# Kernel tuning notes

Hardware: AMD Instinct MI355X
Metric: run time of the kernel (lower is better)

## Reference

```python
import jax, jax.numpy as jnp
import numpy as np

FP8_MAX = 448.0   # max finite value of float8_e4m3fn
GROUP = 128       # quant group size (both act cols and weight blocks)


def fp8_roundtrip(v):
    # Round-to-nearest onto the fp8 e4m3fn grid, back to f32.
    return v.astype(jnp.float8_e4m3fn).astype(jnp.float32)


def setup_inputs() -> dict:
    key = jax.random.key(0)
    k1, k2, k3 = jax.random.split(key, 3)
    M, H = 8192, 4096
    x = jax.random.normal(k1, (M, 2 * H), dtype=jnp.float32)
    # weight: rand -> fp8 grid (stored as f32 values lying exactly on fp8 grid)
    w_q = fp8_roundtrip(jax.random.uniform(k2, (H, H), dtype=jnp.float32))
    # per-(128,128)-block weight scales
    wscale = jax.random.uniform(k3, (H // GROUP, H // GROUP), dtype=jnp.float32)
    return {"x": x, "w_q": w_q, "wscale": wscale}


def reference(x, w_q, wscale):
    H = x.shape[-1] // 2
    # SiluAndMul: silu(gate) * up
    y = jax.nn.silu(x[:, :H]) * x[:, H:]            # [M, H]
    M = y.shape[0]
    # --- activation group quant, group shape (1, 128) ---
    g = y.reshape(M, H // GROUP, GROUP)
    amax = jnp.max(jnp.abs(g), axis=-1, keepdims=True)
    scale = jnp.maximum(amax, 1e-12) / FP8_MAX      # [M, H/128, 1]
    q = fp8_roundtrip(g / scale)                    # fp8-grid values
    y_dq = (q * scale).reshape(M, H)                # dequantized activation
    # --- weight block dequant, block shape (128, 128) ---
    nk, nn = H // GROUP, H // GROUP
    w_dq = (w_q.reshape(nk, GROUP, nn, GROUP) * wscale[:, None, :, None]).reshape(H, H)
    # block-fp8 linear: out[m, n] = sum_k y_dq[m, k] * w_dq[k, n]
    return y_dq @ w_dq
```

## Files before the change

kernel.cpp:

```cpp
#include <hip/hip_runtime.h>
#include <hip/hip_fp8.h>
#include <hip/hip_bf16.h>

#define MDIM 8192
#define HDIM 4096
#define NKT 64

typedef float f32x4 __attribute__((ext_vector_type(4)));
typedef short bf16x8 __attribute__((ext_vector_type(8)));
typedef unsigned short u16x4 __attribute__((ext_vector_type(4)));

__device__ inline void gload_lds16(const void* g, void* l) {
  __builtin_amdgcn_global_load_lds(
      (const __attribute__((address_space(1))) void*)g,
      (__attribute__((address_space(3))) void*)l, 16, 0, 0);
}

__device__ inline unsigned short f2bf(float f) {
  __hip_bfloat16 h = __float2bfloat16(f);
  return *reinterpret_cast<unsigned short*>(&h);
}

__global__ __launch_bounds__(256) void silu_quant_kernel(
    const float* __restrict__ x, unsigned short* __restrict__ yb) {
  const int m = blockIdx.x;
  const int t = threadIdx.x;
  const int g = t >> 3;
  const int i = t & 7;
  const float* xr = x + (size_t)m * (2 * HDIM);

  float v[16];
  float amax = 0.f;
#pragma unroll
  for (int j = 0; j < 4; ++j) {
    const int off = g * 128 + j * 32 + i * 4;
    f32x4 gate = *(const f32x4*)(xr + off);
    f32x4 up = *(const f32x4*)(xr + HDIM + off);
#pragma unroll
    for (int c = 0; c < 4; ++c) {
      float gg = gate[c];
      float s = gg / (1.f + expf(-gg));
      float val = s * up[c];
      v[j * 4 + c] = val;
      amax = fmaxf(amax, fabsf(val));
    }
  }
#pragma unroll
  for (int d = 1; d < 8; d <<= 1) amax = fmaxf(amax, __shfl_xor(amax, d, 64));
  const float scale = fmaxf(amax, 1e-12f) / 448.0f;

#pragma unroll
  for (int j = 0; j < 4; ++j) {
    u16x4 pk;
#pragma unroll
    for (int c = 0; c < 4; ++c) {
      __hip_fp8_e4m3 qv(v[j * 4 + c] / scale);
      pk[c] = f2bf((float)qv * scale);
    }
    *(u16x4*)(yb + (size_t)m * HDIM + g * 128 + j * 32 + i * 4) = pk;
  }
}

__global__ __launch_bounds__(256) void wconv_kernel(
    const float* __restrict__ w, const float* __restrict__ wsc,
    unsigned short* __restrict__ wt) {
  __shared__ unsigned short tile[64][66];
  const int t = threadIdx.x;
  const int n0 = (blockIdx.x & 63) * 64;
  const int k0 = (blockIdx.x >> 6) * 64;
  const float ws = wsc[(k0 >> 7) * 32 + (n0 >> 7)];
  {
    const int r = t >> 4;
    const int c4 = (t & 15) << 2;
#pragma unroll
    for (int j = 0; j < 4; ++j) {
      const int kr = r + j * 16;
      f32x4 vv = *(const f32x4*)(w + (size_t)(k0 + kr) * HDIM + n0 + c4);
#pragma unroll
      for (int c = 0; c < 4; ++c) tile[kr][c4 + c] = f2bf(vv[c] * ws);
    }
  }
  __syncthreads();
  {
    const int n = t >> 4;
    const int k4 = (t & 15) << 2;
#pragma unroll
    for (int j = 0; j < 4; ++j) {
      const int nn = n + j * 16;
      u16x4 pk;
#pragma unroll
      for (int c = 0; c < 4; ++c) pk[c] = tile[k4 + c][nn];
      *(u16x4*)(wt + (size_t)(n0 + nn) * HDIM + k0 + k4) = pk;
    }
  }
}

#define SBAR do { __builtin_amdgcn_sched_barrier(0); __builtin_amdgcn_s_barrier(); __builtin_amdgcn_sched_barrier(0); } while (0)
#define VMW0 asm volatile("s_waitcnt vmcnt(0)" ::: "memory")
#define LGKM0 asm volatile("s_waitcnt lgkmcnt(0)" ::: "memory")

#define STAGE_UNIT(nx, kt, u) do {                                          \
    const __hip_bfloat16* gsrc;  unsigned char* ldst;                       \
    if ((u) == 0)      { gsrc = A + (size_t)(m0 + r0) * HDIM;       ldst = As[nx]; }          \
    else if ((u) == 1) { gsrc = B + (size_t)(n0 + r0) * HDIM;       ldst = Bs[nx]; }          \
    else if ((u) == 2) { gsrc = A + (size_t)(m0 + 128 + r0) * HDIM; ldst = As[nx] + 16384; }  \
    else               { gsrc = B + (size_t)(n0 + 128 + r0) * HDIM; ldst = Bs[nx] + 16384; }  \
    gsrc += (kt) * 64 + cst * 8;                                            \
    gload_lds16(gsrc, ldst + t * 16);                                       \
    gload_lds16(gsrc + (size_t)64 * HDIM, ldst + 8192 + t * 16);            \
  } while (0)

#define STAGE_ALL(nx, kt) do {                                              \
    STAGE_UNIT(nx, kt, 0); STAGE_UNIT(nx, kt, 1);                           \
    STAGE_UNIT(nx, kt, 2); STAGE_UNIT(nx, kt, 3);                           \
    __builtin_amdgcn_sched_barrier(0);                                      \
  } while (0)

#define RD_A(cur, mh) do { _Pragma("unroll") for (int mi = 0; mi < 4; ++mi) { \
    const int row = wm * 128 + (mh) * 64 + mi * 16 + lrow;                    \
    _Pragma("unroll") for (int kk = 0; kk < 2; ++kk)                          \
      afr[mi][kk] = *(const bf16x8*)(As[cur] + row * 128 + (((kk * 4 + lhi) ^ rx) * 16)); \
  } } while (0)

#define RD_B(cur, nh) do { _Pragma("unroll") for (int ni = 0; ni < 2; ++ni) { \
    const int row = wn * 64 + (nh) * 32 + ni * 16 + lrow;                     \
    _Pragma("unroll") for (int kk = 0; kk < 2; ++kk)                          \
      bfr[nh][ni][kk] = *(const bf16x8*)(Bs[cur] + row * 128 + (((kk * 4 + lhi) ^ rx) * 16)); \
  } } while (0)

#define MFMA16(mh, nh) do { _Pragma("unroll") for (int kk = 0; kk < 2; ++kk)  \
    _Pragma("unroll") for (int mi = 0; mi < 4; ++mi)                          \
      _Pragma("unroll") for (int ni = 0; ni < 2; ++ni)                        \
        acc[(mh) * 4 + mi][(nh) * 2 + ni] = __builtin_amdgcn_mfma_f32_16x16x32_bf16( \
            afr[mi][kk], bfr[nh][ni][kk], acc[(mh) * 4 + mi][(nh) * 2 + ni], 0, 0, 0); \
  } while (0)

#define COMPUTE(cur) do {                                                    \
    RD_A(cur, 0); RD_B(cur, 0); RD_B(cur, 1);                                \
    __builtin_amdgcn_s_setprio(1);                                           \
    MFMA16(0, 0); MFMA16(0, 1);                                              \
    __builtin_amdgcn_s_setprio(0);                                           \
    RD_A(cur, 1);                                                            \
    __builtin_amdgcn_s_setprio(1);                                           \
    MFMA16(1, 0); MFMA16(1, 1);                                              \
    __builtin_amdgcn_s_setprio(0);                                           \
  } while (0)

__global__ __launch_bounds__(512, 2) void gemm_bf16_kernel(
    const __hip_bfloat16* __restrict__ A,
    const __hip_bfloat16* __restrict__ B,
    float* __restrict__ out) {
  __shared__ __align__(16) unsigned char As[2][32768];
  __shared__ __align__(16) unsigned char Bs[2][32768];

  const int bid = blockIdx.x;
  const int swz = (bid & 7) * 64 + (bid >> 3);
  const int m0 = (swz & 31) * 256;
  const int n0 = (swz >> 5) * 256;

  const int t = threadIdx.x;
  const int l = t & 63, wid = t >> 6;
  const int wm = wid >> 2, wn = wid & 3;
  const int lrow = l & 15, lhi = l >> 4;
  const int rx = lrow & 7;

  const int r0 = t >> 3;
  const int cst = (t & 7) ^ (r0 & 7);

  f32x4 acc[8][4];
#pragma unroll
  for (int a = 0; a < 8; ++a)
#pragma unroll
    for (int b = 0; b < 4; ++b) acc[a][b] = (f32x4){0.f, 0.f, 0.f, 0.f};
  bf16x8 afr[4][2], bfr[2][2][2];

  STAGE_ALL(0, 0);
  VMW0;
  SBAR;

  int cur = 0;
  for (int kt = 0; kt < NKT - 1; ++kt) {
    const int nx = cur ^ 1;
    STAGE_ALL(nx, kt + 1);
    COMPUTE(cur);
    VMW0;
    LGKM0;
    SBAR;
    cur = nx;
  }
  COMPUTE(cur);

#pragma unroll
  for (int a = 0; a < 8; ++a) {
    const int moff = (a >> 2) * 64 + (a & 3) * 16;
#pragma unroll
    for (int r = 0; r < 4; ++r) {
      const int grow = m0 + wm * 128 + moff + lhi * 4 + r;
      float* orow = out + (size_t)grow * HDIM + n0 + wn * 64 + lrow;
#pragma unroll
      for (int b = 0; b < 4; ++b) {
        const int coff = (b >> 1) * 32 + (b & 1) * 16;
        orow[coff] = acc[a][b][r];
      }
    }
  }
}

extern "C" void kernel_launch(void* const* d_in, const int* in_sizes, int n_in,
                              void* d_out, int out_size, void* d_ws, size_t ws_size,
                              hipStream_t stream) {
  const float* x = (const float*)d_in[0];
  const float* wq = (const float*)d_in[1];
  const float* wsc = (const float*)d_in[2];
  float* out = (float*)d_out;

  unsigned short* yb = (unsigned short*)d_ws;
  unsigned short* wt = yb + (size_t)MDIM * HDIM;

  silu_quant_kernel<<<MDIM, 256, 0, stream>>>(x, yb);
  wconv_kernel<<<(HDIM / 64) * (HDIM / 64), 256, 0, stream>>>(wq, wsc, wt);
  gemm_bf16_kernel<<<(MDIM / 256) * (HDIM / 256), 512, 0, stream>>>(
      (const __hip_bfloat16*)yb, (const __hip_bfloat16*)wt, out);
}
```

Measured before the change: 363.2 us.

## Switch GEMM to 4-stage BK=32 pipeline with partial vmcnt waits

The bf16 GEMM K-tile shrinks from 64 to 32 and the LDS ring grows from 2 to 4 buffers, prefetching three tiles ahead. Waits become vmcnt(8) instead of a full drain, so global loads stay in flight across iterations. The LDS swizzle and the block-to-tile mapping also change to a grouped 8x8 raster for L2 reuse. In exchange there are twice as many barriers per K and smaller MFMA batches per sync, and the LDS footprint per block stays at 128KB, which limits occupancy.

```diff
diff --git a/kernel.cpp b/kernel.cpp
--- a/kernel.cpp
+++ b/kernel.cpp
@@ -4,7 +4,7 @@
 
 #define MDIM 8192
 #define HDIM 4096
-#define NKT 64
+#define NKT 128
 
 typedef float f32x4 __attribute__((ext_vector_type(4)));
 typedef short bf16x8 __attribute__((ext_vector_type(8)));
@@ -96,53 +96,31 @@
 }
 
 #define SBAR do { __builtin_amdgcn_sched_barrier(0); __builtin_amdgcn_s_barrier(); __builtin_amdgcn_sched_barrier(0); } while (0)
-#define VMW0 asm volatile("s_waitcnt vmcnt(0)" ::: "memory")
+#define VMW(n) asm volatile("s_waitcnt vmcnt(" #n ")" ::: "memory")
 #define LGKM0 asm volatile("s_waitcnt lgkmcnt(0)" ::: "memory")
 
-#define STAGE_UNIT(nx, kt, u) do {                                          \
-    const __hip_bfloat16* gsrc;  unsigned char* ldst;                       \
-    if ((u) == 0)      { gsrc = A + (size_t)(m0 + r0) * HDIM;       ldst = As[nx]; }          \
-    else if ((u) == 1) { gsrc = B + (size_t)(n0 + r0) * HDIM;       ldst = Bs[nx]; }          \
-    else if ((u) == 2) { gsrc = A + (size_t)(m0 + 128 + r0) * HDIM; ldst = As[nx] + 16384; }  \
-    else               { gsrc = B + (size_t)(n0 + 128 + r0) * HDIM; ldst = Bs[nx] + 16384; }  \
-    gsrc += (kt) * 64 + cst * 8;                                            \
-    gload_lds16(gsrc, ldst + t * 16);                                       \
-    gload_lds16(gsrc + (size_t)64 * HDIM, ldst + 8192 + t * 16);            \
+#define STAGE(bi, kt) do {                                                   \
+    const __hip_bfloat16* ga = A + aoff + (size_t)(kt) * 32;                 \
+    const __hip_bfloat16* gb = B + boff + (size_t)(kt) * 32;                 \
+    unsigned char* la = As + (bi) * 16384 + t * 16;                          \
+    unsigned char* lb = Bs + (bi) * 16384 + t * 16;                          \
+    gload_lds16(ga, la); gload_lds16(ga + (size_t)128 * HDIM, la + 8192);    \
+    gload_lds16(gb, lb); gload_lds16(gb + (size_t)128 * HDIM, lb + 8192);    \
+    __builtin_amdgcn_sched_barrier(0);                                       \
   } while (0)
 
-#define STAGE_ALL(nx, kt) do {                                              \
-    STAGE_UNIT(nx, kt, 0); STAGE_UNIT(nx, kt, 1);                           \
-    STAGE_UNIT(nx, kt, 2); STAGE_UNIT(nx, kt, 3);                           \
-    __builtin_amdgcn_sched_barrier(0);                                      \
-  } while (0)
-
-#define RD_A(cur, mh) do { _Pragma("unroll") for (int mi = 0; mi < 4; ++mi) { \
-    const int row = wm * 128 + (mh) * 64 + mi * 16 + lrow;                    \
-    _Pragma("unroll") for (int kk = 0; kk < 2; ++kk)                          \
-      afr[mi][kk] = *(const bf16x8*)(As[cur] + row * 128 + (((kk * 4 + lhi) ^ rx) * 16)); \
-  } } while (0)
-
-#define RD_B(cur, nh) do { _Pragma("unroll") for (int ni = 0; ni < 2; ++ni) { \
-    const int row = wn * 64 + (nh) * 32 + ni * 16 + lrow;                     \
-    _Pragma("unroll") for (int kk = 0; kk < 2; ++kk)                          \
-      bfr[nh][ni][kk] = *(const bf16x8*)(Bs[cur] + row * 128 + (((kk * 4 + lhi) ^ rx) * 16)); \
-  } } while (0)
-
-#define MFMA16(mh, nh) do { _Pragma("unroll") for (int kk = 0; kk < 2; ++kk)  \
-    _Pragma("unroll") for (int mi = 0; mi < 4; ++mi)                          \
-      _Pragma("unroll") for (int ni = 0; ni < 2; ++ni)                        \
-        acc[(mh) * 4 + mi][(nh) * 2 + ni] = __builtin_amdgcn_mfma_f32_16x16x32_bf16( \
-            afr[mi][kk], bfr[nh][ni][kk], acc[(mh) * 4 + mi][(nh) * 2 + ni], 0, 0, 0); \
-  } while (0)
-
-#define COMPUTE(cur) do {                                                    \
-    RD_A(cur, 0); RD_B(cur, 0); RD_B(cur, 1);                                \
+#define COMPUTE(bi) do {                                                     \
+    const unsigned char* pa = As + (bi) * 16384;                             \
+    const unsigned char* pb = Bs + (bi) * 16384;                             \
+    _Pragma("unroll") for (int mi = 0; mi < 8; ++mi)                         \
+      afr[mi] = *(const bf16x8*)(pa + (wm * 128 + mi * 16 + lrow) * 64 + cRd * 16); \
+    _Pragma("unroll") for (int ni = 0; ni < 4; ++ni)                         \
+      bfr[ni] = *(const bf16x8*)(pb + (wn * 64 + ni * 16 + lrow) * 64 + cRd * 16);  \
     __builtin_amdgcn_s_setprio(1);                                           \
-    MFMA16(0, 0); MFMA16(0, 1);                                              \
-    __builtin_amdgcn_s_setprio(0);                                           \
-    RD_A(cur, 1);                                                            \
-    __builtin_amdgcn_s_setprio(1);                                           \
-    MFMA16(1, 0); MFMA16(1, 1);                                              \
+    _Pragma("unroll") for (int mi = 0; mi < 8; ++mi)                         \
+      _Pragma("unroll") for (int ni = 0; ni < 4; ++ni)                       \
+        acc[mi][ni] = __builtin_amdgcn_mfma_f32_16x16x32_bf16(               \
+            afr[mi], bfr[ni], acc[mi][ni], 0, 0, 0);                         \
     __builtin_amdgcn_s_setprio(0);                                           \
   } while (0)
 
@@ -150,60 +128,56 @@
     const __hip_bfloat16* __restrict__ A,
     const __hip_bfloat16* __restrict__ B,
     float* __restrict__ out) {
-  __shared__ __align__(16) unsigned char As[2][32768];
-  __shared__ __align__(16) unsigned char Bs[2][32768];
+  __shared__ __align__(16) unsigned char As[4 * 16384];
+  __shared__ __align__(16) unsigned char Bs[4 * 16384];
 
   const int bid = blockIdx.x;
-  const int swz = (bid & 7) * 64 + (bid >> 3);
-  const int m0 = (swz & 31) * 256;
-  const int n0 = (swz >> 5) * 256;
+  const int x = bid & 7, sub = bid >> 3;
+  const int mtile = (x >> 1) * 8 + (sub & 7);
+  const int ntile = (x & 1) * 8 + (sub >> 3);
+  const int m0 = mtile * 256, n0 = ntile * 256;
 
   const int t = threadIdx.x;
   const int l = t & 63, wid = t >> 6;
   const int wm = wid >> 2, wn = wid & 3;
   const int lrow = l & 15, lhi = l >> 4;
-  const int rx = lrow & 7;
+  const int cRd = lhi ^ ((lrow >> 1) & 3);
 
-  const int r0 = t >> 3;
-  const int cst = (t & 7) ^ (r0 & 7);
+  const int cSt = (t & 3) ^ ((t >> 3) & 3);
+  const size_t aoff = (size_t)(m0 + (t >> 2)) * HDIM + cSt * 8;
+  const size_t boff = (size_t)(n0 + (t >> 2)) * HDIM + cSt * 8;
 
   f32x4 acc[8][4];
 #pragma unroll
   for (int a = 0; a < 8; ++a)
 #pragma unroll
     for (int b = 0; b < 4; ++b) acc[a][b] = (f32x4){0.f, 0.f, 0.f, 0.f};
-  bf16x8 afr[4][2], bfr[2][2][2];
+  bf16x8 afr[8], bfr[4];
 
-  STAGE_ALL(0, 0);
-  VMW0;
+  STAGE(0, 0); STAGE(1, 1); STAGE(2, 2);
+  VMW(8);
   SBAR;
 
-  int cur = 0;
-  for (int kt = 0; kt < NKT - 1; ++kt) {
-    const int nx = cur ^ 1;
-    STAGE_ALL(nx, kt + 1);
-    COMPUTE(cur);
-    VMW0;
+  for (int kt = 0; kt < NKT - 3; ++kt) {
+    STAGE((kt + 3) & 3, kt + 3);
+    COMPUTE(kt & 3);
+    VMW(8);
     LGKM0;
     SBAR;
-    cur = nx;
   }
-  COMPUTE(cur);
+  COMPUTE((NKT - 3) & 3); VMW(4); LGKM0; SBAR;
+  COMPUTE((NKT - 2) & 3); VMW(0); LGKM0; SBAR;
+  COMPUTE((NKT - 1) & 3);
 
 #pragma unroll
-  for (int a = 0; a < 8; ++a) {
-    const int moff = (a >> 2) * 64 + (a & 3) * 16;
+  for (int mi = 0; mi < 8; ++mi)
 #pragma unroll
     for (int r = 0; r < 4; ++r) {
-      const int grow = m0 + wm * 128 + moff + lhi * 4 + r;
+      const int grow = m0 + wm * 128 + mi * 16 + lhi * 4 + r;
       float* orow = out + (size_t)grow * HDIM + n0 + wn * 64 + lrow;
 #pragma unroll
-      for (int b = 0; b < 4; ++b) {
-        const int coff = (b >> 1) * 32 + (b & 1) * 16;
-        orow[coff] = acc[a][b][r];
-      }
+      for (int ni = 0; ni < 4; ++ni) orow[ni * 16] = acc[mi][ni][r];
     }
-  }
 }
 
 extern "C" void kernel_launch(void* const* d_in, const int* in_sizes, int n_in,
```

Measured after the change: 393.2 us. +8.3%, slower.
